# Performance work log

Measured on AMD Instinct MI355X. Metric: run time of the kernel, lower is better.

The kernel has to match this reference:

```python
import jax, jax.numpy as jnp
import numpy as np

N_NODES = 100000


def _gcn_norm(edge_index, num_nodes):
    # PyG GCNConv default: add self-loops, symmetric normalization.
    src = jnp.concatenate([edge_index[0], jnp.arange(num_nodes, dtype=edge_index.dtype)])
    dst = jnp.concatenate([edge_index[1], jnp.arange(num_nodes, dtype=edge_index.dtype)])
    deg = jax.ops.segment_sum(jnp.ones_like(dst, dtype=jnp.float32), dst, num_segments=num_nodes)
    dis = jnp.where(deg > 0, jax.lax.rsqrt(deg), 0.0)  # deg^{-1/2}
    norm = dis[src] * dis[dst]  # [E + N]
    return src, dst, norm


def _gcn_conv(x, W, b, src, dst, norm, num_nodes):
    h = x @ W.T                      # [N, out] transform first (out < in)
    msg = h[src] * norm[:, None]     # gather + per-edge scale
    agg = jax.ops.segment_sum(msg, dst, num_segments=num_nodes)  # scatter-add
    return agg + b


def setup_inputs() -> dict:
    key = jax.random.key(0)
    ks = jax.random.split(key, 12)
    E = 3200000
    x = jax.random.normal(ks[0], (N_NODES, 128), dtype=jnp.float32)
    edge_index = jax.random.randint(ks[1], (2, E), 0, N_NODES, dtype=jnp.int64)
    s = lambda k, sh, fan: jax.random.normal(k, sh, dtype=jnp.float32) * (1.0 / np.sqrt(fan))
    return {
        "x": x,
        "edge_index": edge_index,
        "W1": s(ks[2], (32, 128), 128), "b1": jnp.zeros((32,), jnp.float32),
        "W2": s(ks[3], (16, 32), 32),   "b2": jnp.zeros((16,), jnp.float32),
        "w_ih": s(ks[4], (32, 16), 16), "w_hh": s(ks[5], (32, 8), 8),
        "b_ih": s(ks[6], (32,), 8),     "b_hh": s(ks[7], (32,), 8),
        "W_out": s(ks[8], (1, 8), 8),   "b_out": jnp.zeros((1,), jnp.float32),
    }


def reference(x, edge_index, W1, b1, W2, b2, w_ih, w_hh, b_ih, b_hh, W_out, b_out):
    src, dst, norm = _gcn_norm(edge_index, N_NODES)
    h = jax.nn.relu(_gcn_conv(x, W1, b1, src, dst, norm, N_NODES))   # [N, 32]
    h = jax.nn.relu(_gcn_conv(h, W2, b2, src, dst, norm, N_NODES))   # [N, 16]
    # Single-timestep LSTM with h0 = c0 = 0 (gate order: i, f, g, o).
    gates = h @ w_ih.T + b_ih + b_hh   # [N, 32]; h0 @ w_hh.T term is zero
    i, f, g, o = jnp.split(gates, 4, axis=-1)
    c = jax.nn.sigmoid(i) * jnp.tanh(g)
    hh = jax.nn.sigmoid(o) * jnp.tanh(c)  # [N, 8]
    out = hh @ W_out.T + b_out            # [N, 1]
    return out.squeeze(-1)                # [N]
```

## Files before the change

kernel.cpp:

```cpp
#include <hip/hip_runtime.h>
#include <hip/hip_fp16.h>
#include <math.h>

static constexpr int N = 100000;
static constexpr int SHIFT = 7;
static constexpr int BUCKN = 1 << SHIFT;
static constexpr int NBUCK = (N + BUCKN - 1) >> SHIFT;
static constexpr int HDRS  = NBUCK + 1;
static constexpr int CHUNK = 8192;
static constexpr int BPMAX = 512;
static constexpr int STRIDE = 5120;
static constexpr int COLCAP = NBUCK * STRIDE;
static constexpr int ES_CAP = STRIDE;

__device__ __forceinline__ int block_scan_incl(int v, int* wtot, int t) {
    const int lane = t & 63, wv = t >> 6;
    int x = v;
#pragma unroll
    for (int o = 1; o < 64; o <<= 1) {
        int y = __shfl_up(x, o, 64);
        if (lane >= o) x += y;
    }
    __syncthreads();
    if (lane == 63) wtot[wv] = x;
    __syncthreads();
    if (t < 16) {
        int y = wtot[t];
#pragma unroll
        for (int o = 1; o < 16; o <<= 1) {
            int z = __shfl_up(y, o, 16);
            if (t >= o) y += z;
        }
        wtot[t] = y;
    }
    __syncthreads();
    return x + (wv ? wtot[wv - 1] : 0);
}

__global__ __launch_bounds__(1024) void k_part(const int* __restrict__ src,
                                               const int* __restrict__ dst,
                                               int* __restrict__ col,
                                               int* __restrict__ hdr, int E) {
    __shared__ int stage[CHUNK];
    __shared__ int hl[NBUCK];
    __shared__ int cur[NBUCK];
    __shared__ int wtot[16];
    const int t = threadIdx.x, b = blockIdx.x;
    if (t < NBUCK) hl[t] = 0;
    __syncthreads();
    const int e0 = b * CHUNK;
    const int m = min(CHUNK, E - e0);
    for (int i = t; i < m; i += 1024) atomicAdd(&hl[dst[e0 + i] >> SHIFT], 1);
    __syncthreads();
    const int v = (t < NBUCK) ? hl[t] : 0;
    const int inc = block_scan_incl(v, wtot, t);
    if (t < NBUCK) {
        int excl = inc - v;
        cur[t] = excl;
        hdr[b * HDRS + t] = excl;
    }
    if (t == 0) hdr[b * HDRS + NBUCK] = m;
    __syncthreads();
    for (int i = t; i < m; i += 1024) {
        int d = dst[e0 + i];
        int pos = atomicAdd(&cur[d >> SHIFT], 1);
        pos = min(max(pos, 0), CHUNK - 1);
        stage[pos] = (src[e0 + i] & 0x1FFFF) | ((d & (BUCKN - 1)) << 17);
    }
    __syncthreads();
    for (int i = t; i < m; i += 1024) col[e0 + i] = stage[i];
}

__global__ __launch_bounds__(1024) void k_sort(const int* __restrict__ col,
                                               const int* __restrict__ hdr,
                                               int* __restrict__ col2,
                                               int* __restrict__ deg,
                                               int* __restrict__ row_start, int BP) {
    __shared__ int es[ES_CAP];
    __shared__ int rlen[BPMAX];
    __shared__ int rst[BPMAX];
    __shared__ int roff[BPMAX];
    __shared__ int cnt[BUCKN];
    __shared__ int cur[BUCKN];
    __shared__ int wtot[16];
    __shared__ int ntot;
    const int t = threadIdx.x, buck = blockIdx.x;
    if (t < BPMAX) { rlen[t] = 0; rst[t] = 0; }
    __syncthreads();
    if (t < BP) {
        int a = hdr[t * HDRS + buck];
        int e = hdr[t * HDRS + buck + 1];
        rst[t] = min(max(a, 0), CHUNK);
        rlen[t] = min(max(e - a, 0), CHUNK);
    }
    __syncthreads();
    {
        const int v = (t < BPMAX) ? rlen[t] : 0;
        const int inc = block_scan_incl(v, wtot, t);
        if (t < BPMAX) roff[t] = inc - v;
        if (t == 1023) ntot = min(inc, ES_CAP);
    }
    __syncthreads();
    const int n = ntot;
    {
        const int g = t >> 4, l = t & 15;
        for (int r = g; r < BP; r += 64) {
            const int len = rlen[r];
            const int base = r * CHUNK + rst[r];
            const int o = roff[r];
            for (int k = l; k < len; k += 16) {
                int p = o + k;
                if (p < ES_CAP) es[p] = col[base + k];
            }
        }
    }
    __syncthreads();
    if (t < BUCKN) cnt[t] = 0;
    __syncthreads();
    for (int i = t; i < n; i += 1024) atomicAdd(&cnt[(es[i] >> 17) & (BUCKN - 1)], 1);
    __syncthreads();
    {
        const int v = (t < BUCKN) ? cnt[t] : 0;
        const int inc = block_scan_incl(v, wtot, t);
        if (t < BUCKN) {
            int excl = inc - v;
            int node = buck * BUCKN + t;
            if (node < N) {
                deg[node] = v;
                row_start[node] = buck * STRIDE + excl;
            }
            cur[t] = excl;
        }
    }
    __syncthreads();
    for (int i = t; i < n; i += 1024) {
        int p = es[i];
        int pos = atomicAdd(&cur[(p >> 17) & (BUCKN - 1)], 1);
        pos = min(max(pos, 0), STRIDE - 1);
        col2[buck * STRIDE + pos] = p & 0x1FFFF;
    }
}

__global__ __launch_bounds__(256) void k_xw1(
        const float* __restrict__ x, const float* __restrict__ W1,
        const int* __restrict__ deg, __half* __restrict__ g1h) {
    __shared__ float4 wtv[32 * 33];
    __shared__ float4 xsv[1024];
    const int t = threadIdx.x;
    const float4* W1v = (const float4*)W1;
    for (int idx = t; idx < 1024; idx += 256) {
        int j = idx >> 5, kb = idx & 31;
        wtv[kb * 33 + j] = W1v[idx];
    }
    const float4* x4 = (const float4*)x + (size_t)blockIdx.x * 1024;
    for (int idx = t; idx < 1024; idx += 256) xsv[idx] = x4[idx];
    __syncthreads();

    const int j = t & 31, ng = t >> 5;
    float a0 = 0.f, a1 = 0.f, a2 = 0.f, a3 = 0.f;
#pragma unroll 4
    for (int kb = 0; kb < 32; ++kb) {
        float4 w = wtv[kb * 33 + j];
        float4 x0 = xsv[(4 * ng + 0) * 32 + kb];
        float4 x1 = xsv[(4 * ng + 1) * 32 + kb];
        float4 x2 = xsv[(4 * ng + 2) * 32 + kb];
        float4 x3 = xsv[(4 * ng + 3) * 32 + kb];
        a0 = fmaf(w.x, x0.x, fmaf(w.y, x0.y, fmaf(w.z, x0.z, fmaf(w.w, x0.w, a0))));
        a1 = fmaf(w.x, x1.x, fmaf(w.y, x1.y, fmaf(w.z, x1.z, fmaf(w.w, x1.w, a1))));
        a2 = fmaf(w.x, x2.x, fmaf(w.y, x2.y, fmaf(w.z, x2.z, fmaf(w.w, x2.w, a2))));
        a3 = fmaf(w.x, x3.x, fmaf(w.y, x3.y, fmaf(w.z, x3.z, fmaf(w.w, x3.w, a3))));
    }
    const int nb = blockIdx.x * 32 + 4 * ng;
    g1h[(nb + 0) * 32 + j] = __float2half(a0 * rsqrtf((float)(deg[nb + 0] + 1)));
    g1h[(nb + 1) * 32 + j] = __float2half(a1 * rsqrtf((float)(deg[nb + 1] + 1)));
    g1h[(nb + 2) * 32 + j] = __float2half(a2 * rsqrtf((float)(deg[nb + 2] + 1)));
    g1h[(nb + 3) * 32 + j] = __float2half(a3 * rsqrtf((float)(deg[nb + 3] + 1)));
}

__global__ __launch_bounds__(256) void k_gather1(
        const int* __restrict__ row_start, const int* __restrict__ deg,
        const int* __restrict__ col2, const __half* __restrict__ g1h,
        const float* __restrict__ b1, const float* __restrict__ W2,
        __half* __restrict__ g2h) {
    __shared__ float h1s[64 * 33];
    __shared__ float w2t[32 * 17];
    const int t = threadIdx.x;
    for (int idx = t; idx < 512; idx += 256) {
        int j = idx >> 5, k = idx & 31;
        w2t[k * 17 + j] = W2[idx];
    }
    const int lane = t & 63, w = t >> 6;
    const int q = lane & 3;
    const int nloc = w * 16 + (lane >> 2);
    const int node = blockIdx.x * 64 + nloc;
    const int nc = node < N ? node : N - 1;
    const int rs = row_start[nc];
    const int ne = (node < N) ? deg[nc] : 0;
    const uint4* g1v = (const uint4*)g1h;

    float acc[8];
    {
        uint4 rv = g1v[nc * 4 + q];
        const __half2* hp = (const __half2*)&rv;
#pragma unroll
        for (int m2 = 0; m2 < 4; ++m2) {
            float2 f = __half22float2(hp[m2]);
            acc[2 * m2] = f.x;
            acc[2 * m2 + 1] = f.y;
        }
    }
    int svN[4];
#pragma unroll
    for (int c = 0; c < 4; ++c)
        svN[c] = (4 * c + q < ne) ? col2[rs + 4 * c + q] : 0;
    for (int base = 0; base < ne; base += 16) {
        int sv[4];
#pragma unroll
        for (int c = 0; c < 4; ++c) sv[c] = svN[c];
        const int nb2 = base + 16;
        if (nb2 < ne) {
#pragma unroll
            for (int c = 0; c < 4; ++c)
                svN[c] = (nb2 + 4 * c + q < ne) ? col2[rs + nb2 + 4 * c + q] : 0;
        }
        int idx[16];
#pragma unroll
        for (int c = 0; c < 4; ++c)
#pragma unroll
            for (int u = 0; u < 4; ++u)
                idx[4 * c + u] = min(__shfl(sv[c], u, 4), N - 1);
        uint4 rv[16];
#pragma unroll
        for (int u = 0; u < 16; ++u) rv[u] = g1v[idx[u] * 4 + q];
#pragma unroll
        for (int u = 0; u < 16; ++u) {
            float wt = (base + u < ne) ? 1.f : 0.f;
            const __half2* hp = (const __half2*)&rv[u];
#pragma unroll
            for (int m2 = 0; m2 < 4; ++m2) {
                float2 f = __half22float2(hp[m2]);
                acc[2 * m2]     = fmaf(wt, f.x, acc[2 * m2]);
                acc[2 * m2 + 1] = fmaf(wt, f.y, acc[2 * m2 + 1]);
            }
        }
    }
    {
        const float dis = rsqrtf((float)(ne + 1));
#pragma unroll
        for (int u = 0; u < 8; ++u) {
            float v = (node < N) ? (acc[u] * dis + b1[q * 8 + u]) : 0.f;
            h1s[nloc * 33 + q * 8 + u] = v > 0.f ? v : 0.f;
        }
    }
    __syncthreads();
    const int n2 = t >> 2, jq = (t & 3) * 4;
    const int node2 = blockIdx.x * 64 + n2;
    if (node2 < N) {
        float a0 = 0.f, a1 = 0.f, a2 = 0.f, a3 = 0.f;
        const float* hr = h1s + n2 * 33;
#pragma unroll
        for (int k = 0; k < 32; ++k) {
            float h = hr[k];
            a0 = fmaf(h, w2t[k * 17 + jq + 0], a0);
            a1 = fmaf(h, w2t[k * 17 + jq + 1], a1);
            a2 = fmaf(h, w2t[k * 17 + jq + 2], a2);
            a3 = fmaf(h, w2t[k * 17 + jq + 3], a3);
        }
        const float dis2 = rsqrtf((float)(deg[node2] + 1));
        __half2* g2p = (__half2*)(g2h + node2 * 16 + jq);
        g2p[0] = __floats2half2_rn(a0 * dis2, a1 * dis2);
        g2p[1] = __floats2half2_rn(a2 * dis2, a3 * dis2);
    }
}

__global__ __launch_bounds__(256) void k_gather2(
        const int* __restrict__ row_start, const int* __restrict__ deg,
        const int* __restrict__ col2, const __half* __restrict__ g2h,
        const float* __restrict__ b2, float* __restrict__ h2) {
    const int t = threadIdx.x;
    const int lane = t & 63, w = t >> 6;
    const int q = lane & 1;
    const int node = blockIdx.x * 128 + w * 32 + (lane >> 1);
    const int nc = node < N ? node : N - 1;
    const int rs = row_start[nc];
    const int ne = (node < N) ? deg[nc] : 0;
    const uint4* g2v = (const uint4*)g2h;

    float acc[8];
    {
        uint4 rv = g2v[nc * 2 + q];
        const __half2* hp = (const __half2*)&rv;
#pragma unroll
        for (int m2 = 0; m2 < 4; ++m2) {
            float2 f = __half22float2(hp[m2]);
            acc[2 * m2] = f.x;
            acc[2 * m2 + 1] = f.y;
        }
    }
    int svN[8];
#pragma unroll
    for (int c = 0; c < 8; ++c)
        svN[c] = (2 * c + q < ne) ? col2[rs + 2 * c + q] : 0;
    for (int base = 0; base < ne; base += 16) {
        int sv[8];
#pragma unroll
        for (int c = 0; c < 8; ++c) sv[c] = svN[c];
        const int nb2 = base + 16;
        if (nb2 < ne) {
#pragma unroll
            for (int c = 0; c < 8; ++c)
                svN[c] = (nb2 + 2 * c + q < ne) ? col2[rs + nb2 + 2 * c + q] : 0;
        }
        int idx[16];
#pragma unroll
        for (int c = 0; c < 8; ++c) {
            idx[2 * c]     = min(__shfl(sv[c], 0, 2), N - 1);
            idx[2 * c + 1] = min(__shfl(sv[c], 1, 2), N - 1);
        }
        uint4 rv[16];
#pragma unroll
        for (int u = 0; u < 16; ++u) rv[u] = g2v[idx[u] * 2 + q];
#pragma unroll
        for (int u = 0; u < 16; ++u) {
            float wt = (base + u < ne) ? 1.f : 0.f;
            const __half2* hp = (const __half2*)&rv[u];
#pragma unroll
            for (int m2 = 0; m2 < 4; ++m2) {
                float2 f = __half22float2(hp[m2]);
                acc[2 * m2]     = fmaf(wt, f.x, acc[2 * m2]);
                acc[2 * m2 + 1] = fmaf(wt, f.y, acc[2 * m2 + 1]);
            }
        }
    }
    if (node < N) {
        const float dis = rsqrtf((float)(ne + 1));
        float4* h2v = (float4*)h2;
#pragma unroll
        for (int h = 0; h < 2; ++h) {
            float4 o;
            float v0 = acc[4 * h + 0] * dis + b2[q * 8 + 4 * h + 0];
            float v1 = acc[4 * h + 1] * dis + b2[q * 8 + 4 * h + 1];
            float v2 = acc[4 * h + 2] * dis + b2[q * 8 + 4 * h + 2];
            float v3 = acc[4 * h + 3] * dis + b2[q * 8 + 4 * h + 3];
            o.x = v0 > 0.f ? v0 : 0.f;
            o.y = v1 > 0.f ? v1 : 0.f;
            o.z = v2 > 0.f ? v2 : 0.f;
            o.w = v3 > 0.f ? v3 : 0.f;
            h2v[node * 4 + q * 2 + h] = o;
        }
    }
}

__global__ __launch_bounds__(256) void k_final(
        const float* __restrict__ h2g,
        const float* __restrict__ w_ih, const float* __restrict__ b_ih,
        const float* __restrict__ b_hh, const float* __restrict__ W_out,
        const float* __restrict__ b_out, float* __restrict__ out) {
    __shared__ float wih[512];
    __shared__ float bias[32];
    __shared__ float wout[8];
    __shared__ float bo;
    const int t = threadIdx.x;
    for (int idx = t; idx < 512; idx += 256) wih[idx] = w_ih[idx];
    if (t < 32) bias[t] = b_ih[t] + b_hh[t];
    if (t < 8)  wout[t] = W_out[t];
    if (t == 0) bo = b_out[0];
    __syncthreads();

    const int i = blockIdx.x * 256 + t;
    if (i >= N) return;
    float h2[16];
    const float4* a4 = (const float4*)(h2g + (size_t)i * 16);
#pragma unroll
    for (int q = 0; q < 4; ++q) {
        float4 v = a4[q];
        h2[q * 4 + 0] = v.x; h2[q * 4 + 1] = v.y;
        h2[q * 4 + 2] = v.z; h2[q * 4 + 3] = v.w;
    }
    float oacc = 0.f;
#pragma unroll
    for (int q = 0; q < 8; ++q) {
        float gi = bias[q], gg = bias[16 + q], go = bias[24 + q];
#pragma unroll
        for (int k = 0; k < 16; ++k) {
            gi = fmaf(h2[k], wih[q * 16 + k], gi);
            gg = fmaf(h2[k], wih[(16 + q) * 16 + k], gg);
            go = fmaf(h2[k], wih[(24 + q) * 16 + k], go);
        }
        float c  = (1.f / (1.f + expf(-gi))) * tanhf(gg);
        float hh = (1.f / (1.f + expf(-go))) * tanhf(c);
        oacc = fmaf(hh, wout[q], oacc);
    }
    out[i] = oacc + bo;
}

extern "C" void kernel_launch(void* const* d_in, const int* in_sizes, int n_in,
                              void* d_out, int out_size, void* d_ws, size_t ws_size,
                              hipStream_t stream) {
    const float* x     = (const float*)d_in[0];
    const int*   ei    = (const int*)d_in[1];
    const float* W1    = (const float*)d_in[2];
    const float* b1    = (const float*)d_in[3];
    const float* W2    = (const float*)d_in[4];
    const float* b2    = (const float*)d_in[5];
    const float* w_ih  = (const float*)d_in[6];
    const float* b_ih  = (const float*)d_in[8];
    const float* b_hh  = (const float*)d_in[9];
    const float* W_out = (const float*)d_in[10];
    const float* b_out = (const float*)d_in[11];
    float* out = (float*)d_out;

    const int E = in_sizes[1] / 2;
    const int* src = ei;
    const int* dst = ei + E;
    int BP = (E + CHUNK - 1) / CHUNK;
    if (BP > BPMAX) BP = BPMAX;

    int* col       = (int*)d_ws;
    int* hdr       = col + (size_t)BPMAX * CHUNK;
    int* col2      = hdr + (size_t)BPMAX * HDRS;
    int* deg       = col2 + COLCAP;
    int* row_start = deg + N;
    int* base2     = row_start + N;
    __half* g1h    = (__half*)base2;
    __half* g2h    = (__half*)(base2 + (size_t)N * 16);
    float* h2      = (float*)(base2 + (size_t)N * 24);

    k_part   <<<BP,              1024, 0, stream>>>(src, dst, col, hdr, E);
    k_sort   <<<NBUCK,           1024, 0, stream>>>(col, hdr, col2, deg, row_start, BP);
    k_xw1    <<<N / 32,          256,  0, stream>>>(x, W1, deg, g1h);
    k_gather1<<<(N + 63) / 64,   256,  0, stream>>>(row_start, deg, col2, g1h, b1, W2, g2h);
    k_gather2<<<(N + 127) / 128, 256,  0, stream>>>(row_start, deg, col2, g2h, b2, h2);
    k_final  <<<(N + 255) / 256, 256,  0, stream>>>(h2, w_ih, b_ih, b_hh, W_out, b_out, out);
}
```

Measured before the change: 246.1 us.

## Fuse LSTM head into second gather and vectorize partition loads

Folds the final LSTM/output kernel into the second-layer gather. Each lane pair computes partial gate dot products over its 8 features and combines them with a lane shuffle, so the h2 intermediate buffer and one kernel launch disappear. The partition kernel also switches to int4 loads for src/dst and int4 stores from the staging buffer, cutting the number of memory instructions. In exchange, the gather kernel takes on extra shared-memory setup and gate arithmetic that is duplicated across lane pairs.

```diff
diff --git a/kernel.cpp b/kernel.cpp
--- a/kernel.cpp
+++ b/kernel.cpp
@@ -41,7 +41,7 @@
                                                const int* __restrict__ dst,
                                                int* __restrict__ col,
                                                int* __restrict__ hdr, int E) {
-    __shared__ int stage[CHUNK];
+    __shared__ __align__(16) int stage[CHUNK];
     __shared__ int hl[NBUCK];
     __shared__ int cur[NBUCK];
     __shared__ int wtot[16];
@@ -50,7 +50,16 @@
     __syncthreads();
     const int e0 = b * CHUNK;
     const int m = min(CHUNK, E - e0);
-    for (int i = t; i < m; i += 1024) atomicAdd(&hl[dst[e0 + i] >> SHIFT], 1);
+    const int m4 = m >> 2;
+    const int4* d4 = (const int4*)(dst + e0);
+    for (int i = t; i < m4; i += 1024) {
+        int4 d = d4[i];
+        atomicAdd(&hl[d.x >> SHIFT], 1);
+        atomicAdd(&hl[d.y >> SHIFT], 1);
+        atomicAdd(&hl[d.z >> SHIFT], 1);
+        atomicAdd(&hl[d.w >> SHIFT], 1);
+    }
+    for (int i = (m4 << 2) + t; i < m; i += 1024) atomicAdd(&hl[dst[e0 + i] >> SHIFT], 1);
     __syncthreads();
     const int v = (t < NBUCK) ? hl[t] : 0;
     const int inc = block_scan_incl(v, wtot, t);
@@ -61,14 +70,31 @@
     }
     if (t == 0) hdr[b * HDRS + NBUCK] = m;
     __syncthreads();
-    for (int i = t; i < m; i += 1024) {
+    const int4* s4 = (const int4*)(src + e0);
+    for (int i = t; i < m4; i += 1024) {
+        int4 d = d4[i];
+        int4 s = s4[i];
+        int p;
+        p = atomicAdd(&cur[d.x >> SHIFT], 1); p = min(max(p, 0), CHUNK - 1);
+        stage[p] = (s.x & 0x1FFFF) | ((d.x & (BUCKN - 1)) << 17);
+        p = atomicAdd(&cur[d.y >> SHIFT], 1); p = min(max(p, 0), CHUNK - 1);
+        stage[p] = (s.y & 0x1FFFF) | ((d.y & (BUCKN - 1)) << 17);
+        p = atomicAdd(&cur[d.z >> SHIFT], 1); p = min(max(p, 0), CHUNK - 1);
+        stage[p] = (s.z & 0x1FFFF) | ((d.z & (BUCKN - 1)) << 17);
+        p = atomicAdd(&cur[d.w >> SHIFT], 1); p = min(max(p, 0), CHUNK - 1);
+        stage[p] = (s.w & 0x1FFFF) | ((d.w & (BUCKN - 1)) << 17);
+    }
+    for (int i = (m4 << 2) + t; i < m; i += 1024) {
         int d = dst[e0 + i];
-        int pos = atomicAdd(&cur[d >> SHIFT], 1);
-        pos = min(max(pos, 0), CHUNK - 1);
-        stage[pos] = (src[e0 + i] & 0x1FFFF) | ((d & (BUCKN - 1)) << 17);
-    }
-    __syncthreads();
-    for (int i = t; i < m; i += 1024) col[e0 + i] = stage[i];
+        int p = atomicAdd(&cur[d >> SHIFT], 1);
+        p = min(max(p, 0), CHUNK - 1);
+        stage[p] = (src[e0 + i] & 0x1FFFF) | ((d & (BUCKN - 1)) << 17);
+    }
+    __syncthreads();
+    int4* c4 = (int4*)(col + e0);
+    const int4* st4 = (const int4*)stage;
+    for (int i = t; i < m4; i += 1024) c4[i] = st4[i];
+    for (int i = (m4 << 2) + t; i < m; i += 1024) col[e0 + i] = stage[i];
 }
 
 __global__ __launch_bounds__(1024) void k_sort(const int* __restrict__ col,
@@ -276,8 +302,21 @@
 __global__ __launch_bounds__(256) void k_gather2(
         const int* __restrict__ row_start, const int* __restrict__ deg,
         const int* __restrict__ col2, const __half* __restrict__ g2h,
-        const float* __restrict__ b2, float* __restrict__ h2) {
+        const float* __restrict__ b2,
+        const float* __restrict__ w_ih, const float* __restrict__ b_ih,
+        const float* __restrict__ b_hh, const float* __restrict__ W_out,
+        const float* __restrict__ b_out, float* __restrict__ out) {
+    __shared__ __align__(16) float wihs[512];
+    __shared__ float bias[32];
+    __shared__ float wout[8];
+    __shared__ float bo;
     const int t = threadIdx.x;
+    for (int idx = t; idx < 512; idx += 256) wihs[idx] = w_ih[idx];
+    if (t < 32) bias[t] = b_ih[t] + b_hh[t];
+    if (t < 8)  wout[t] = W_out[t];
+    if (t == 0) bo = b_out[0];
+    __syncthreads();
+
     const int lane = t & 63, w = t >> 6;
     const int q = lane & 1;
     const int node = blockIdx.x * 128 + w * 32 + (lane >> 1);
@@ -332,66 +371,35 @@
             }
         }
     }
-    if (node < N) {
+    {
         const float dis = rsqrtf((float)(ne + 1));
-        float4* h2v = (float4*)h2;
-#pragma unroll
-        for (int h = 0; h < 2; ++h) {
-            float4 o;
-            float v0 = acc[4 * h + 0] * dis + b2[q * 8 + 4 * h + 0];
-            float v1 = acc[4 * h + 1] * dis + b2[q * 8 + 4 * h + 1];
-            float v2 = acc[4 * h + 2] * dis + b2[q * 8 + 4 * h + 2];
-            float v3 = acc[4 * h + 3] * dis + b2[q * 8 + 4 * h + 3];
-            o.x = v0 > 0.f ? v0 : 0.f;
-            o.y = v1 > 0.f ? v1 : 0.f;
-            o.z = v2 > 0.f ? v2 : 0.f;
-            o.w = v3 > 0.f ? v3 : 0.f;
-            h2v[node * 4 + q * 2 + h] = o;
-        }
-    }
-}
-
-__global__ __launch_bounds__(256) void k_final(
-        const float* __restrict__ h2g,
-        const float* __restrict__ w_ih, const float* __restrict__ b_ih,
-        const float* __restrict__ b_hh, const float* __restrict__ W_out,
-        const float* __restrict__ b_out, float* __restrict__ out) {
-    __shared__ float wih[512];
-    __shared__ float bias[32];
-    __shared__ float wout[8];
-    __shared__ float bo;
-    const int t = threadIdx.x;
-    for (int idx = t; idx < 512; idx += 256) wih[idx] = w_ih[idx];
-    if (t < 32) bias[t] = b_ih[t] + b_hh[t];
-    if (t < 8)  wout[t] = W_out[t];
-    if (t == 0) bo = b_out[0];
-    __syncthreads();
-
-    const int i = blockIdx.x * 256 + t;
-    if (i >= N) return;
-    float h2[16];
-    const float4* a4 = (const float4*)(h2g + (size_t)i * 16);
-#pragma unroll
-    for (int q = 0; q < 4; ++q) {
-        float4 v = a4[q];
-        h2[q * 4 + 0] = v.x; h2[q * 4 + 1] = v.y;
-        h2[q * 4 + 2] = v.z; h2[q * 4 + 3] = v.w;
-    }
+#pragma unroll
+        for (int u = 0; u < 8; ++u) {
+            float v = acc[u] * dis + b2[q * 8 + u];
+            acc[u] = v > 0.f ? v : 0.f;
+        }
+    }
+    const float4* w4 = (const float4*)wihs;
     float oacc = 0.f;
 #pragma unroll
-    for (int q = 0; q < 8; ++q) {
-        float gi = bias[q], gg = bias[16 + q], go = bias[24 + q];
-#pragma unroll
-        for (int k = 0; k < 16; ++k) {
-            gi = fmaf(h2[k], wih[q * 16 + k], gi);
-            gg = fmaf(h2[k], wih[(16 + q) * 16 + k], gg);
-            go = fmaf(h2[k], wih[(24 + q) * 16 + k], go);
-        }
+    for (int g = 0; g < 8; ++g) {
+        float4 wi0 = w4[g * 4 + q * 2],        wi1 = w4[g * 4 + q * 2 + 1];
+        float4 wg0 = w4[(16 + g) * 4 + q * 2], wg1 = w4[(16 + g) * 4 + q * 2 + 1];
+        float4 wo0 = w4[(24 + g) * 4 + q * 2], wo1 = w4[(24 + g) * 4 + q * 2 + 1];
+        float gi = acc[0] * wi0.x + acc[1] * wi0.y + acc[2] * wi0.z + acc[3] * wi0.w
+                 + acc[4] * wi1.x + acc[5] * wi1.y + acc[6] * wi1.z + acc[7] * wi1.w;
+        float gg = acc[0] * wg0.x + acc[1] * wg0.y + acc[2] * wg0.z + acc[3] * wg0.w
+                 + acc[4] * wg1.x + acc[5] * wg1.y + acc[6] * wg1.z + acc[7] * wg1.w;
+        float go = acc[0] * wo0.x + acc[1] * wo0.y + acc[2] * wo0.z + acc[3] * wo0.w
+                 + acc[4] * wo1.x + acc[5] * wo1.y + acc[6] * wo1.z + acc[7] * wo1.w;
+        gi = gi + __shfl_xor(gi, 1, 2) + bias[g];
+        gg = gg + __shfl_xor(gg, 1, 2) + bias[16 + g];
+        go = go + __shfl_xor(go, 1, 2) + bias[24 + g];
         float c  = (1.f / (1.f + expf(-gi))) * tanhf(gg);
         float hh = (1.f / (1.f + expf(-go))) * tanhf(c);
-        oacc = fmaf(hh, wout[q], oacc);
-    }
-    out[i] = oacc + bo;
+        oacc = fmaf(hh, wout[g], oacc);
+    }
+    if (node < N && q == 0) out[node] = oacc + bo;
 }
 
 extern "C" void kernel_launch(void* const* d_in, const int* in_sizes, int n_in,
@@ -424,12 +432,11 @@
     int* base2     = row_start + N;
     __half* g1h    = (__half*)base2;
     __half* g2h    = (__half*)(base2 + (size_t)N * 16);
-    float* h2      = (float*)(base2 + (size_t)N * 24);
 
     k_part   <<<BP,              1024, 0, stream>>>(src, dst, col, hdr, E);
     k_sort   <<<NBUCK,           1024, 0, stream>>>(col, hdr, col2, deg, row_start, BP);
     k_xw1    <<<N / 32,          256,  0, stream>>>(x, W1, deg, g1h);
     k_gather1<<<(N + 63) / 64,   256,  0, stream>>>(row_start, deg, col2, g1h, b1, W2, g2h);
-    k_gather2<<<(N + 127) / 128, 256,  0, stream>>>(row_start, deg, col2, g2h, b2, h2);
-    k_final  <<<(N + 255) / 256, 256,  0, stream>>>(h2, w_ih, b_ih, b_hh, W_out, b_out, out);
-}
+    k_gather2<<<(N + 127) / 128, 256,  0, stream>>>(row_start, deg, col2, g2h, b2,
+                                                    w_ih, b_ih, b_hh, W_out, b_out, out);
+}
```

After: 239.4 us. 1.03x faster.
